# Kernel optimization log

Hardware: AMD Instinct MI355X
Metric: run time of the kernel (lower is better)

## Reference

```python
import jax, jax.numpy as jnp
import numpy as np

H = 768
F = 3072
NH = 12
EPS = 1e-5


def _layer_norm(x, g, b):
    mu = jnp.mean(x, axis=-1, keepdims=True)
    var = jnp.mean(jnp.square(x - mu), axis=-1, keepdims=True)
    return (x - mu) * jax.lax.rsqrt(var + EPS) * g + b


def setup_inputs() -> dict:
    key = jax.random.key(0)
    ks = jax.random.split(key, 16)
    s = 0.02
    d = {
        'x': jax.random.normal(ks[0], (2, 2048, H), jnp.float32),
        'Wq': jax.random.normal(ks[1], (H, H), jnp.float32) * s,
        'bq': jnp.zeros((H,), jnp.float32),
        'Wk': jax.random.normal(ks[2], (H, H), jnp.float32) * s,
        'bk': jnp.zeros((H,), jnp.float32),
        'Wv': jax.random.normal(ks[3], (H, H), jnp.float32) * s,
        'bv': jnp.zeros((H,), jnp.float32),
        'Wa1': jax.random.normal(ks[4], (H, H), jnp.float32) * s,
        'ba1': jnp.zeros((H,), jnp.float32),
        'g1': jnp.ones((H,), jnp.float32),
        'be1': jnp.zeros((H,), jnp.float32),
        'W1': jax.random.normal(ks[5], (H, F), jnp.float32) * s,
        'b1': jnp.zeros((F,), jnp.float32),
        'W2': jax.random.normal(ks[6], (F, H), jnp.float32) * s,
        'b2': jnp.zeros((H,), jnp.float32),
        'Wa2': jax.random.normal(ks[7], (H, H), jnp.float32) * s,
        'ba2': jnp.zeros((H,), jnp.float32),
        'g2': jnp.ones((H,), jnp.float32),
        'be2': jnp.zeros((H,), jnp.float32),
    }
    return d


def reference(x, Wq, bq, Wk, bk, Wv, bv, Wa1, ba1, g1, be1, W1, b1, W2, b2, Wa2, ba2, g2, be2):
    B, S, _ = x.shape
    Dh = H // NH
    # multi-head attention (naive: explicit scores + softmax)
    q = (x @ Wq + bq).reshape(B, S, NH, Dh)
    k = (x @ Wk + bk).reshape(B, S, NH, Dh)
    v = (x @ Wv + bv).reshape(B, S, NH, Dh)
    scores = jnp.einsum('bqhd,bkhd->bhqk', q, k) / jnp.sqrt(jnp.float32(Dh))
    att = jax.nn.softmax(scores, axis=-1)
    ctx = jnp.einsum('bhqk,bkhd->bqhd', att, v).reshape(B, S, H)
    # add_norm_1: Linear -> LayerNorm, then residual added AFTER LN (as in source)
    an1 = _layer_norm(ctx @ Wa1 + ba1, g1, be1) + x
    # feed-forward with exact GELU (torch nn.GELU default)
    ff = jax.nn.gelu(an1 @ W1 + b1, approximate=False) @ W2 + b2
    # add_norm_2: Linear -> LayerNorm, residual after LN
    out = _layer_norm(ff @ Wa2 + ba2, g2, be2) + an1
    return out
```

## Files before the change

kernel.cpp:

```cpp
#include <hip/hip_runtime.h>
#include <stdint.h>
#include <stddef.h>

#define HD 768
#define FF 3072
#define NHEAD 12
#define DHEAD 64
#define SEQ 2048
#define BATCH 2
#define NTOK (SEQ*BATCH)
#define SM_SCALE 0.18033688f

typedef __attribute__((ext_vector_type(8))) __bf16 bf16x8;
typedef __attribute__((ext_vector_type(4))) float f32x4;

__device__ __forceinline__ unsigned short f2bf(float f) {
  unsigned int u = __builtin_bit_cast(unsigned int, f);
  u += 0x7fffu + ((u >> 16) & 1u);
  return (unsigned short)(u >> 16);
}
__device__ __forceinline__ float bf2f(unsigned int s) {
  unsigned int u = s << 16;
  return __builtin_bit_cast(float, u);
}
__device__ __forceinline__ float4 ld4bf(const unsigned short* p) {
  uint2 w = *reinterpret_cast<const uint2*>(p);
  float4 o;
  o.x = bf2f(w.x & 0xffffu); o.y = bf2f(w.x >> 16);
  o.z = bf2f(w.y & 0xffffu); o.w = bf2f(w.y >> 16);
  return o;
}

__device__ __forceinline__ void gl16(const unsigned short* g, unsigned short* l) {
  __builtin_amdgcn_global_load_lds(
      (const __attribute__((address_space(1))) void*)g,
      (__attribute__((address_space(3))) void*)l,
      16, 0, 0);
}

__global__ void k_prep(const float* __restrict__ Wq, const float* __restrict__ Wk,
                       const float* __restrict__ Wv, const float* __restrict__ Wa1,
                       const float* __restrict__ W1, const float* __restrict__ W2,
                       const float* __restrict__ Wa2,
                       unsigned short* __restrict__ WqkvT, unsigned short* __restrict__ Wa1T,
                       unsigned short* __restrict__ W1T, unsigned short* __restrict__ W2T,
                       unsigned short* __restrict__ Wa2T,
                       const float* __restrict__ x, unsigned short* __restrict__ xb, int n4,
                       const float* __restrict__ bq, const float* __restrict__ bk,
                       const float* __restrict__ bv, float* __restrict__ biasqkv) {
  int t = blockIdx.x;
  int tid = threadIdx.x;
  if (t >= 7488) {
    int tb = t - 7488;
    if (tb < 9) {
      int idx = tb * 256 + tid;
      if (idx < 3*HD) {
        float v = idx < HD ? bq[idx] : idx < 2*HD ? bk[idx-HD] : bv[idx-2*HD];
        biasqkv[idx] = v;
      }
    }
    int i = tb * 256 + tid;
    int stride = 2048 * 256;
    for (; i < n4; i += stride) {
      float4 v = reinterpret_cast<const float4*>(x)[i];
      ushort4 o;
      o.x = f2bf(v.x); o.y = f2bf(v.y); o.z = f2bf(v.z); o.w = f2bf(v.w);
      reinterpret_cast<ushort4*>(xb)[i] = o;
    }
    return;
  }
  __shared__ float tile[32][33];
  const float* in; unsigned short* out; int K, N;
  if (t < 2304)      { int seg = t / 576; t -= seg * 576; K = HD; N = HD;
                       in  = seg==0 ? Wq : seg==1 ? Wk : seg==2 ? Wv : Wa1;
                       out = seg<3 ? WqkvT + seg*HD*HD : Wa1T; }
  else if (t < 4608) { t -= 2304; in = W1;  out = W1T;  K = HD; N = FF; }
  else if (t < 6912) { t -= 4608; in = W2;  out = W2T;  K = FF; N = HD; }
  else               { t -= 6912; in = Wa2; out = Wa2T; K = HD; N = HD; }
  int nt = N / 32;
  int nb = (t % nt) * 32, kb = (t / nt) * 32;
  int tx = tid & 31, ty = tid >> 5;
  for (int i = ty; i < 32; i += 8)
    tile[i][tx] = in[(size_t)(kb + i) * N + nb + tx];
  __syncthreads();
  for (int i = ty; i < 32; i += 8)
    out[(size_t)(nb + i) * K + kb + tx] = f2bf(tile[tx][i]);
}


#define BN 128
#define BK 64

template<int MODE, int TBM>
__global__ __launch_bounds__(256, 3)
void k_gemm(const unsigned short* __restrict__ A, const unsigned short* __restrict__ Bt,
            const float* __restrict__ bias, void* __restrict__ Cout,
            unsigned short* __restrict__ Vout,
            int M, int N, int K) {
  constexpr int MR = TBM / 32;
  constexpr int AI = TBM / 32;
  __shared__ unsigned short As[TBM*BK];
  __shared__ unsigned short Bs[BN*BK];
  int tid = threadIdx.x;
  int nwg = gridDim.x * gridDim.y;
  int lin = blockIdx.x + gridDim.x * blockIdx.y;
  int nl = (lin & 7) * (nwg >> 3) + (lin >> 3);
  int bm = (nl % gridDim.x) * TBM;
  int bn = (nl / gridDim.x) * BN;
  int wave = tid >> 6, lane = tid & 63;
  int wm = wave >> 1, wn = wave & 1;
  int wr = wm * (TBM/2);
  int wc = wn * 64;
  int fr = lane & 15;
  int hi = lane >> 4;

  f32x4 acc[MR][4];
#pragma unroll
  for (int m = 0; m < MR; ++m)
#pragma unroll
    for (int n = 0; n < 4; ++n) acc[m][n] = (f32x4){0.f,0.f,0.f,0.f};

  int g8 = lane >> 3;
  int cc = (lane & 7) ^ g8;
  int arow = (TBM/4)*wave + g8;
  int brow = 32*wave + g8;
  const unsigned short* ag = A + (size_t)(bm + arow) * K + cc*8;
  const unsigned short* bg = Bt + (size_t)(bn + brow) * K + cc*8;
  unsigned short* asl = As + (TBM/4)*wave*BK;
  unsigned short* bsl = Bs + 32*wave*BK;

  for (int k0 = 0; k0 < K; k0 += BK) {
#pragma unroll
    for (int i = 0; i < AI; ++i)
      gl16(ag + (size_t)(8*i)*K + k0, asl + (8*i)*BK);
#pragma unroll
    for (int i = 0; i < 4; ++i)
      gl16(bg + (size_t)(8*i)*K + k0, bsl + (8*i)*BK);
    __syncthreads();

    bf16x8 af[MR][2], bf[4][2];
#pragma unroll
    for (int m = 0; m < MR; ++m) {
      int R = wr + m*16 + fr, sw = R & 7;
#pragma unroll
      for (int h2 = 0; h2 < 2; ++h2)
        af[m][h2] = __builtin_bit_cast(bf16x8,
          *reinterpret_cast<const uint4*>(&As[R*BK + ((hi + h2*4) ^ sw)*8]));
    }
#pragma unroll
    for (int n = 0; n < 4; ++n) {
      int R = wc + n*16 + fr, sw = R & 7;
#pragma unroll
      for (int h2 = 0; h2 < 2; ++h2)
        bf[n][h2] = __builtin_bit_cast(bf16x8,
          *reinterpret_cast<const uint4*>(&Bs[R*BK + ((hi + h2*4) ^ sw)*8]));
    }
#pragma unroll
    for (int m = 0; m < MR; ++m)
#pragma unroll
      for (int n = 0; n < 4; ++n) {
        acc[m][n] = __builtin_amdgcn_mfma_f32_16x16x32_bf16(af[m][0], bf[n][0], acc[m][n], 0, 0, 0);
        acc[m][n] = __builtin_amdgcn_mfma_f32_16x16x32_bf16(af[m][1], bf[n][1], acc[m][n], 0, 0, 0);
      }
    __syncthreads();
  }

  int crow0 = (lane >> 4) * 4;
  int ccol = lane & 15;

  if (MODE == 3 && bn >= 2*HD) {
    unsigned short* tb = (wave < 2) ? As + wave*4096 : Bs + (wave-2)*4096;
#pragma unroll
    for (int m = 0; m < MR; ++m)
#pragma unroll
      for (int n = 0; n < 4; ++n)
#pragma unroll
        for (int r = 0; r < 4; ++r) {
          int tl = m*16 + crow0 + r;
          int cl = n*16 + ccol;
          float v = acc[m][n][r] + bias[bn + wc + cl];
          int pt = ((tl>>2)&3)*16 + ((tl>>4)<<2) + (tl&3);
          tb[cl*64 + (((pt>>3) ^ (cl&7))<<3) + (pt&7)] = f2bf(v);
        }
    __syncthreads();
    int tk0 = bm + wr;
    int bb = tk0 >> 11;
    int sb = tk0 & 2047;
    int hh = (bn + wc - 2*HD) >> 6;
    unsigned short* dst = Vout + ((size_t)(bb*NHEAD + hh) * DHEAD) * SEQ + sb;
#pragma unroll
    for (int p = 0; p < 8; ++p) {
      int dr = p*8 + (lane >> 3);
      int cj = lane & 7;
      uint4 w = *reinterpret_cast<const uint4*>(&tb[dr*64 + ((cj ^ (dr&7))<<3)]);
      *reinterpret_cast<uint4*>(dst + (size_t)dr*SEQ + cj*8) = w;
    }
    return;
  }

#pragma unroll
  for (int m = 0; m < MR; ++m) {
#pragma unroll
    for (int n = 0; n < 4; ++n) {
      int gcol = bn + wc + n*16 + ccol;
      float bv_ = bias[gcol];
#pragma unroll
      for (int r = 0; r < 4; ++r) {
        int grow = bm + wr + m*16 + crow0 + r;
        float v = acc[m][n][r] + bv_;
        if (MODE == 2) {
          float a = v + 0.044715f * v * v * v;
          v = v / (1.0f + exp2f(-2.3022082f * a));
        }
        if (MODE == 3 && gcol < HD) v *= SM_SCALE;
        reinterpret_cast<unsigned short*>(Cout)[(size_t)grow * N + gcol] = f2bf(v);
      }
    }
  }
}


#define KVB 128
#define KPK 72
#define KPV 136

__global__ __launch_bounds__(256, 3)
void k_attn_mfma(const unsigned short* __restrict__ qkv,
                 const unsigned short* __restrict__ vt,
                 unsigned short* __restrict__ ctx) {
  __shared__ __align__(16) char smem[40960];
  auto Ks = reinterpret_cast<unsigned short(*)[KPK]>(smem);
  auto Vt = reinterpret_cast<unsigned short(*)[KPV]>(smem + 18432);
  auto Mg = reinterpret_cast<f32x4(*)[64]>(smem);

  int tid = threadIdx.x;
  int wv = tid >> 6, lane = tid & 63;
  int lo = lane & 15, hi = lane >> 4;
  int qh = wv & 1;
  int kh = wv >> 1;

  int lin = blockIdx.x + 32*(blockIdx.y + NHEAD*blockIdx.z);
  int nl = (lin & 7) * 96 + (lin >> 3);
  int qb = nl & 31;
  int rest = nl >> 5;
  int h = rest % NHEAD;
  int b = rest / NHEAD;
  int q0 = qb * 64;

  for (int idx = tid; idx < 16*KPV; idx += 256) {
    int rr = idx / KPV, cc2 = idx - rr*KPV;
    Vt[64 + rr][cc2] = (rr == 0) ? (unsigned short)0x3F80 : (unsigned short)0;
  }

  const unsigned short* qpA = qkv + (size_t)(b*SEQ + q0 + qh*32 + lo) * 2304 + h*DHEAD + hi*8;
  const unsigned short* qpB = qpA + (size_t)16 * 2304;
  bf16x8 qfA0 = __builtin_bit_cast(bf16x8, *reinterpret_cast<const uint4*>(qpA));
  bf16x8 qfA1 = __builtin_bit_cast(bf16x8, *reinterpret_cast<const uint4*>(qpA + 32));
  bf16x8 qfB0 = __builtin_bit_cast(bf16x8, *reinterpret_cast<const uint4*>(qpB));
  bf16x8 qfB1 = __builtin_bit_cast(bf16x8, *reinterpret_cast<const uint4*>(qpB + 32));

  f32x4 poA[4], poB[4], po5A, po5B;
#pragma unroll
  for (int dt = 0; dt < 4; ++dt) { poA[dt] = (f32x4){0.f,0.f,0.f,0.f}; poB[dt] = (f32x4){0.f,0.f,0.f,0.f}; }
  po5A = (f32x4){0.f,0.f,0.f,0.f};
  po5B = (f32x4){0.f,0.f,0.f,0.f};

  int ksr = tid >> 1, kc = (tid & 1) * 32;
  int vdr = tid >> 2, vc = (tid & 3) * 32;
  const unsigned short* kgl = qkv + (size_t)(b*SEQ)*2304 + HD + h*DHEAD;
  const unsigned short* vgl = vt + ((size_t)(b*NHEAD + h)) * DHEAD * SEQ;

  for (int t0 = 0; t0 < SEQ; t0 += KVB) {
    const unsigned short* kp = kgl + (size_t)(t0 + ksr)*2304 + kc;
    const unsigned short* vp = vgl + (size_t)vdr*SEQ + t0 + vc;
    uint4 ku0 = *reinterpret_cast<const uint4*>(kp);
    uint4 ku1 = *reinterpret_cast<const uint4*>(kp + 8);
    uint4 ku2 = *reinterpret_cast<const uint4*>(kp + 16);
    uint4 ku3 = *reinterpret_cast<const uint4*>(kp + 24);
    uint4 vu0 = *reinterpret_cast<const uint4*>(vp);
    uint4 vu1 = *reinterpret_cast<const uint4*>(vp + 8);
    uint4 vu2 = *reinterpret_cast<const uint4*>(vp + 16);
    uint4 vu3 = *reinterpret_cast<const uint4*>(vp + 24);
    __syncthreads();
    *reinterpret_cast<uint4*>(&Ks[ksr][kc])      = ku0;
    *reinterpret_cast<uint4*>(&Ks[ksr][kc + 8])  = ku1;
    *reinterpret_cast<uint4*>(&Ks[ksr][kc + 16]) = ku2;
    *reinterpret_cast<uint4*>(&Ks[ksr][kc + 24]) = ku3;
    *reinterpret_cast<uint4*>(&Vt[vdr][vc])      = vu0;
    *reinterpret_cast<uint4*>(&Vt[vdr][vc + 8])  = vu1;
    *reinterpret_cast<uint4*>(&Vt[vdr][vc + 16]) = vu2;
    *reinterpret_cast<uint4*>(&Vt[vdr][vc + 24]) = vu3;
    __syncthreads();

    f32x4 sA[4], sB[4];
#pragma unroll
    for (int kg = 0; kg < 4; ++kg) {
      int krow = kh*64 + kg*16 + lo;
      bf16x8 a0 = __builtin_bit_cast(bf16x8, *reinterpret_cast<const uint4*>(&Ks[krow][hi*8]));
      bf16x8 a1 = __builtin_bit_cast(bf16x8, *reinterpret_cast<const uint4*>(&Ks[krow][32 + hi*8]));
      f32x4 s = (f32x4){0.f,0.f,0.f,0.f};
      s = __builtin_amdgcn_mfma_f32_16x16x32_bf16(a0, qfA0, s, 0, 0, 0);
      s = __builtin_amdgcn_mfma_f32_16x16x32_bf16(a1, qfA1, s, 0, 0, 0);
      sA[kg] = s;
      s = (f32x4){0.f,0.f,0.f,0.f};
      s = __builtin_amdgcn_mfma_f32_16x16x32_bf16(a0, qfB0, s, 0, 0, 0);
      s = __builtin_amdgcn_mfma_f32_16x16x32_bf16(a1, qfB1, s, 0, 0, 0);
      sB[kg] = s;
    }

    unsigned int pwA[8], pwB[8];
#pragma unroll
    for (int kg = 0; kg < 4; ++kg) {
      float a0 = exp2f(sA[kg][0]), a1 = exp2f(sA[kg][1]);
      float a2 = exp2f(sA[kg][2]), a3 = exp2f(sA[kg][3]);
      asm("v_cvt_pk_bf16_f32 %0, %1, %2" : "=v"(pwA[kg*2])   : "v"(a0), "v"(a1));
      asm("v_cvt_pk_bf16_f32 %0, %1, %2" : "=v"(pwA[kg*2+1]) : "v"(a2), "v"(a3));
      float b0 = exp2f(sB[kg][0]), b1 = exp2f(sB[kg][1]);
      float b2 = exp2f(sB[kg][2]), b3 = exp2f(sB[kg][3]);
      asm("v_cvt_pk_bf16_f32 %0, %1, %2" : "=v"(pwB[kg*2])   : "v"(b0), "v"(b1));
      asm("v_cvt_pk_bf16_f32 %0, %1, %2" : "=v"(pwB[kg*2+1]) : "v"(b2), "v"(b3));
    }

    uint4 uA0; uA0.x = pwA[0]; uA0.y = pwA[1]; uA0.z = pwA[2]; uA0.w = pwA[3];
    uint4 uA1; uA1.x = pwA[4]; uA1.y = pwA[5]; uA1.z = pwA[6]; uA1.w = pwA[7];
    uint4 uB0; uB0.x = pwB[0]; uB0.y = pwB[1]; uB0.z = pwB[2]; uB0.w = pwB[3];
    uint4 uB1; uB1.x = pwB[4]; uB1.y = pwB[5]; uB1.z = pwB[6]; uB1.w = pwB[7];
    bf16x8 paA0 = __builtin_bit_cast(bf16x8, uA0);
    bf16x8 paA1 = __builtin_bit_cast(bf16x8, uA1);
    bf16x8 paB0 = __builtin_bit_cast(bf16x8, uB0);
    bf16x8 paB1 = __builtin_bit_cast(bf16x8, uB1);

#pragma unroll
    for (int dt = 0; dt < 4; ++dt) {
      int col = dt*16 + lo;
      bf16x8 v0 = __builtin_bit_cast(bf16x8, *reinterpret_cast<const uint4*>(&Vt[col][kh*64 + hi*16]));
      bf16x8 v1 = __builtin_bit_cast(bf16x8, *reinterpret_cast<const uint4*>(&Vt[col][kh*64 + hi*16 + 8]));
      poA[dt] = __builtin_amdgcn_mfma_f32_16x16x32_bf16(paA0, v0, poA[dt], 0, 0, 0);
      poA[dt] = __builtin_amdgcn_mfma_f32_16x16x32_bf16(paA1, v1, poA[dt], 0, 0, 0);
      poB[dt] = __builtin_amdgcn_mfma_f32_16x16x32_bf16(paB0, v0, poB[dt], 0, 0, 0);
      poB[dt] = __builtin_amdgcn_mfma_f32_16x16x32_bf16(paB1, v1, poB[dt], 0, 0, 0);
    }
    {
      bf16x8 o0 = __builtin_bit_cast(bf16x8, *reinterpret_cast<const uint4*>(&Vt[64 + lo][kh*64 + hi*16]));
      bf16x8 o1 = __builtin_bit_cast(bf16x8, *reinterpret_cast<const uint4*>(&Vt[64 + lo][kh*64 + hi*16 + 8]));
      po5A = __builtin_amdgcn_mfma_f32_16x16x32_bf16(paA0, o0, po5A, 0, 0, 0);
      po5A = __builtin_amdgcn_mfma_f32_16x16x32_bf16(paA1, o1, po5A, 0, 0, 0);
      po5B = __builtin_amdgcn_mfma_f32_16x16x32_bf16(paB0, o0, po5B, 0, 0, 0);
      po5B = __builtin_amdgcn_mfma_f32_16x16x32_bf16(paB1, o1, po5B, 0, 0, 0);
    }
  }

  __syncthreads();
  if (kh == 1) {
#pragma unroll
    for (int dt = 0; dt < 4; ++dt) {
      Mg[qh*10 + dt][lane] = poA[dt];
      Mg[qh*10 + 4 + dt][lane] = poB[dt];
    }
    Mg[qh*10 + 8][lane] = po5A;
    Mg[qh*10 + 9][lane] = po5B;
  }
  __syncthreads();
  if (kh == 0) {
#pragma unroll
    for (int dt = 0; dt < 4; ++dt) {
      f32x4 mA = Mg[qh*10 + dt][lane], mB = Mg[qh*10 + 4 + dt][lane];
      poA[dt][0] += mA[0]; poA[dt][1] += mA[1]; poA[dt][2] += mA[2]; poA[dt][3] += mA[3];
      poB[dt][0] += mB[0]; poB[dt][1] += mB[1]; poB[dt][2] += mB[2]; poB[dt][3] += mB[3];
    }
    f32x4 m5A = Mg[qh*10 + 8][lane], m5B = Mg[qh*10 + 9][lane];
    po5A[0] += m5A[0]; po5A[1] += m5A[1]; po5A[2] += m5A[2]; po5A[3] += m5A[3];
    po5B[0] += m5B[0]; po5B[1] += m5B[1]; po5B[2] += m5B[2]; po5B[3] += m5B[3];

    unsigned short* op = ctx + (size_t)(b*SEQ + q0 + qh*32) * HD + h*DHEAD;
#pragma unroll
    for (int r = 0; r < 4; ++r) {
      float LA = __shfl(po5A[r], hi*16);
      float LB = __shfl(po5B[r], hi*16);
      float liA = (LA > 0.f) ? 1.0f / LA : 0.f;
      float liB = (LB > 0.f) ? 1.0f / LB : 0.f;
      int row = hi*4 + r;
#pragma unroll
      for (int dt = 0; dt < 4; ++dt) {
        op[(size_t)row*HD + dt*16 + lo]        = f2bf(poA[dt][r] * liA);
        op[(size_t)(16 + row)*HD + dt*16 + lo] = f2bf(poB[dt][r] * liB);
      }
    }
  }
}

template<int RESID_BF16, int WRITE_F32>
__global__ __launch_bounds__(256, 4)
void k_ln(const unsigned short* __restrict__ xin, const void* __restrict__ resid_,
          const float* __restrict__ g, const float* __restrict__ be,
          float* __restrict__ outf, unsigned short* __restrict__ outb) {
  int wave = threadIdx.x >> 6, lane = threadIdx.x & 63;
  int row = blockIdx.x * 4 + wave;
  const unsigned short* xp = xin + (size_t)row * HD;
  const float4* gp = reinterpret_cast<const float4*>(g);
  const float4* bp = reinterpret_cast<const float4*>(be);
  float4 v[3];
  float sum = 0.f, sq = 0.f;
#pragma unroll
  for (int i = 0; i < 3; ++i) {
    v[i] = ld4bf(xp + (lane + 64*i)*4);
    sum += v[i].x + v[i].y + v[i].z + v[i].w;
    sq  += v[i].x*v[i].x + v[i].y*v[i].y + v[i].z*v[i].z + v[i].w*v[i].w;
  }
#pragma unroll
  for (int m = 1; m < 64; m <<= 1) { sum += __shfl_xor(sum, m); sq += __shfl_xor(sq, m); }
  float mean = sum * (1.0f/768.0f);
  float var = sq * (1.0f/768.0f) - mean*mean;
  float rstd = rsqrtf(var + 1e-5f);
#pragma unroll
  for (int i = 0; i < 3; ++i) {
    float4 gg = gp[lane + 64*i], bb = bp[lane + 64*i];
    float4 rr;
    if (RESID_BF16)
      rr = ld4bf((const unsigned short*)resid_ + (size_t)row * HD + (lane + 64*i)*4);
    else
      rr = reinterpret_cast<const float4*>((const float*)resid_ + (size_t)row * HD)[lane + 64*i];
    float4 o;
    o.x = (v[i].x - mean)*rstd*gg.x + bb.x + rr.x;
    o.y = (v[i].y - mean)*rstd*gg.y + bb.y + rr.y;
    o.z = (v[i].z - mean)*rstd*gg.z + bb.z + rr.z;
    o.w = (v[i].w - mean)*rstd*gg.w + bb.w + rr.w;
    if (WRITE_F32) {
      reinterpret_cast<float4*>(outf + (size_t)row * HD)[lane + 64*i] = o;
    } else {
      ushort4 ob;
      ob.x = f2bf(o.x); ob.y = f2bf(o.y); ob.z = f2bf(o.z); ob.w = f2bf(o.w);
      reinterpret_cast<ushort4*>(outb + (size_t)row * HD)[lane + 64*i] = ob;
    }
  }
}


extern "C" void kernel_launch(void* const* d_in, const int* in_sizes, int n_in,
                              void* d_out, int out_size, void* d_ws, size_t ws_size,
                              hipStream_t stream) {
  const float* x   = (const float*)d_in[0];
  const float* Wq  = (const float*)d_in[1];
  const float* bq  = (const float*)d_in[2];
  const float* Wk  = (const float*)d_in[3];
  const float* bk  = (const float*)d_in[4];
  const float* Wv  = (const float*)d_in[5];
  const float* bv  = (const float*)d_in[6];
  const float* Wa1 = (const float*)d_in[7];
  const float* ba1 = (const float*)d_in[8];
  const float* g1  = (const float*)d_in[9];
  const float* be1 = (const float*)d_in[10];
  const float* W1  = (const float*)d_in[11];
  const float* b1  = (const float*)d_in[12];
  const float* W2  = (const float*)d_in[13];
  const float* b2  = (const float*)d_in[14];
  const float* Wa2 = (const float*)d_in[15];
  const float* ba2 = (const float*)d_in[16];
  const float* g2  = (const float*)d_in[17];
  const float* be2 = (const float*)d_in[18];

  char* ws = (char*)d_ws;
  size_t off = 0;
  auto alloc = [&](size_t bytes) -> void* {
    void* p = ws + off;
    off += (bytes + 255) & ~(size_t)255;
    return p;
  };
  unsigned short* xb    = (unsigned short*)alloc((size_t)NTOK*HD*2);
  unsigned short* WqkvT = (unsigned short*)alloc((size_t)3*HD*HD*2);
  unsigned short* Wa1T  = (unsigned short*)alloc((size_t)HD*HD*2);
  unsigned short* W1T   = (unsigned short*)alloc((size_t)FF*HD*2);
  unsigned short* W2T   = (unsigned short*)alloc((size_t)HD*FF*2);
  unsigned short* Wa2T  = (unsigned short*)alloc((size_t)HD*HD*2);
  float*          biasqkv = (float*)alloc((size_t)3*HD*4);
  unsigned short* qkvb  = (unsigned short*)alloc((size_t)NTOK*3*HD*2);
  unsigned short* vtb   = (unsigned short*)alloc((size_t)NTOK*HD*2);
  unsigned short* ctxb  = (unsigned short*)alloc((size_t)NTOK*HD*2);
  unsigned short* a1b   = (unsigned short*)alloc((size_t)NTOK*HD*2);
  unsigned short* an1b  = (unsigned short*)alloc((size_t)NTOK*HD*2);
  unsigned short* h1g   = (unsigned short*)alloc((size_t)NTOK*FF*2);
  unsigned short* f2b   = (unsigned short*)alloc((size_t)NTOK*HD*2);
  unsigned short* a2b   = (unsigned short*)alloc((size_t)NTOK*HD*2);
  (void)ws_size; (void)in_sizes; (void)n_in; (void)out_size;

  k_prep<<<9536, 256, 0, stream>>>(Wq, Wk, Wv, Wa1, W1, W2, Wa2,
                                   WqkvT, Wa1T, W1T, W2T, Wa2T,
                                   x, xb, NTOK*HD/4, bq, bk, bv, biasqkv);

  k_gemm<3,128><<<dim3(NTOK/128, 2304/BN), 256, 0, stream>>>(xb, WqkvT, biasqkv, qkvb, vtb, NTOK, 3*HD, HD);
  k_attn_mfma<<<dim3(SEQ/64, NHEAD, BATCH), 256, 0, stream>>>(qkvb, vtb, ctxb);
  k_gemm<1,64><<<dim3(NTOK/64, HD/BN), 256, 0, stream>>>(ctxb, Wa1T, ba1, a1b, nullptr, NTOK, HD, HD);
  k_ln<0,0><<<NTOK/4, 256, 0, stream>>>(a1b, x, g1, be1, nullptr, an1b);
  k_gemm<2,128><<<dim3(NTOK/128, FF/BN), 256, 0, stream>>>(an1b, W1T, b1, h1g, nullptr, NTOK, FF, HD);
  k_gemm<1,64><<<dim3(NTOK/64, HD/BN), 256, 0, stream>>>(h1g, W2T, b2, f2b, nullptr, NTOK, HD, FF);
  k_gemm<1,64><<<dim3(NTOK/64, HD/BN), 256, 0, stream>>>(f2b, Wa2T, ba2, a2b, nullptr, NTOK, HD, HD);
  k_ln<1,1><<<NTOK/4, 256, 0, stream>>>(a2b, an1b, g2, be2, (float*)d_out, nullptr);
}
```

Before: 189.9 us.

## Give each attention wave its own query rows over full KV tile

The attention kernel now assigns each of the four waves 32 distinct query rows (128 queries per block), and each wave walks both 64-key halves of every KV tile itself. Previously two waves split the keys and had to merge partial outputs through shared memory. This removes the cross-wave reduction and its barriers, and halves how often each K/V tile is loaded per query. The cost is half as many blocks (384), which may leave the GPU's compute units underfilled, plus twice the per-wave work inside each tile.

```diff
diff --git a/kernel.cpp b/kernel.cpp
--- a/kernel.cpp
+++ b/kernel.cpp
@@ -228,31 +228,28 @@
 void k_attn_mfma(const unsigned short* __restrict__ qkv,
                  const unsigned short* __restrict__ vt,
                  unsigned short* __restrict__ ctx) {
-  __shared__ __align__(16) char smem[40960];
+  __shared__ __align__(16) char smem[40192];
   auto Ks = reinterpret_cast<unsigned short(*)[KPK]>(smem);
   auto Vt = reinterpret_cast<unsigned short(*)[KPV]>(smem + 18432);
-  auto Mg = reinterpret_cast<f32x4(*)[64]>(smem);
 
   int tid = threadIdx.x;
   int wv = tid >> 6, lane = tid & 63;
   int lo = lane & 15, hi = lane >> 4;
-  int qh = wv & 1;
-  int kh = wv >> 1;
-
-  int lin = blockIdx.x + 32*(blockIdx.y + NHEAD*blockIdx.z);
-  int nl = (lin & 7) * 96 + (lin >> 3);
-  int qb = nl & 31;
-  int rest = nl >> 5;
+
+  int lin = blockIdx.x + 16*(blockIdx.y + NHEAD*blockIdx.z);
+  int nl = (lin & 7) * 48 + (lin >> 3);
+  int qb = nl & 15;
+  int rest = nl >> 4;
   int h = rest % NHEAD;
   int b = rest / NHEAD;
-  int q0 = qb * 64;
+  int q0 = qb * 128;
 
   for (int idx = tid; idx < 16*KPV; idx += 256) {
     int rr = idx / KPV, cc2 = idx - rr*KPV;
     Vt[64 + rr][cc2] = (rr == 0) ? (unsigned short)0x3F80 : (unsigned short)0;
   }
 
-  const unsigned short* qpA = qkv + (size_t)(b*SEQ + q0 + qh*32 + lo) * 2304 + h*DHEAD + hi*8;
+  const unsigned short* qpA = qkv + (size_t)(b*SEQ + q0 + wv*32 + lo) * 2304 + h*DHEAD + hi*8;
   const unsigned short* qpB = qpA + (size_t)16 * 2304;
   bf16x8 qfA0 = __builtin_bit_cast(bf16x8, *reinterpret_cast<const uint4*>(qpA));
   bf16x8 qfA1 = __builtin_bit_cast(bf16x8, *reinterpret_cast<const uint4*>(qpA + 32));
@@ -292,99 +289,79 @@
     *reinterpret_cast<uint4*>(&Vt[vdr][vc + 24]) = vu3;
     __syncthreads();
 
-    f32x4 sA[4], sB[4];
-#pragma unroll
-    for (int kg = 0; kg < 4; ++kg) {
-      int krow = kh*64 + kg*16 + lo;
-      bf16x8 a0 = __builtin_bit_cast(bf16x8, *reinterpret_cast<const uint4*>(&Ks[krow][hi*8]));
-      bf16x8 a1 = __builtin_bit_cast(bf16x8, *reinterpret_cast<const uint4*>(&Ks[krow][32 + hi*8]));
-      f32x4 s = (f32x4){0.f,0.f,0.f,0.f};
-      s = __builtin_amdgcn_mfma_f32_16x16x32_bf16(a0, qfA0, s, 0, 0, 0);
-      s = __builtin_amdgcn_mfma_f32_16x16x32_bf16(a1, qfA1, s, 0, 0, 0);
-      sA[kg] = s;
-      s = (f32x4){0.f,0.f,0.f,0.f};
-      s = __builtin_amdgcn_mfma_f32_16x16x32_bf16(a0, qfB0, s, 0, 0, 0);
-      s = __builtin_amdgcn_mfma_f32_16x16x32_bf16(a1, qfB1, s, 0, 0, 0);
-      sB[kg] = s;
-    }
-
-    unsigned int pwA[8], pwB[8];
-#pragma unroll
-    for (int kg = 0; kg < 4; ++kg) {
-      float a0 = exp2f(sA[kg][0]), a1 = exp2f(sA[kg][1]);
-      float a2 = exp2f(sA[kg][2]), a3 = exp2f(sA[kg][3]);
-      asm("v_cvt_pk_bf16_f32 %0, %1, %2" : "=v"(pwA[kg*2])   : "v"(a0), "v"(a1));
-      asm("v_cvt_pk_bf16_f32 %0, %1, %2" : "=v"(pwA[kg*2+1]) : "v"(a2), "v"(a3));
-      float b0 = exp2f(sB[kg][0]), b1 = exp2f(sB[kg][1]);
-      float b2 = exp2f(sB[kg][2]), b3 = exp2f(sB[kg][3]);
-      asm("v_cvt_pk_bf16_f32 %0, %1, %2" : "=v"(pwB[kg*2])   : "v"(b0), "v"(b1));
-      asm("v_cvt_pk_bf16_f32 %0, %1, %2" : "=v"(pwB[kg*2+1]) : "v"(b2), "v"(b3));
-    }
-
-    uint4 uA0; uA0.x = pwA[0]; uA0.y = pwA[1]; uA0.z = pwA[2]; uA0.w = pwA[3];
-    uint4 uA1; uA1.x = pwA[4]; uA1.y = pwA[5]; uA1.z = pwA[6]; uA1.w = pwA[7];
-    uint4 uB0; uB0.x = pwB[0]; uB0.y = pwB[1]; uB0.z = pwB[2]; uB0.w = pwB[3];
-    uint4 uB1; uB1.x = pwB[4]; uB1.y = pwB[5]; uB1.z = pwB[6]; uB1.w = pwB[7];
-    bf16x8 paA0 = __builtin_bit_cast(bf16x8, uA0);
-    bf16x8 paA1 = __builtin_bit_cast(bf16x8, uA1);
-    bf16x8 paB0 = __builtin_bit_cast(bf16x8, uB0);
-    bf16x8 paB1 = __builtin_bit_cast(bf16x8, uB1);
-
+#pragma unroll
+    for (int hh = 0; hh < 2; ++hh) {
+      f32x4 sA[4], sB[4];
+#pragma unroll
+      for (int kg = 0; kg < 4; ++kg) {
+        int krow = hh*64 + kg*16 + lo;
+        bf16x8 a0 = __builtin_bit_cast(bf16x8, *reinterpret_cast<const uint4*>(&Ks[krow][hi*8]));
+        bf16x8 a1 = __builtin_bit_cast(bf16x8, *reinterpret_cast<const uint4*>(&Ks[krow][32 + hi*8]));
+        f32x4 s = (f32x4){0.f,0.f,0.f,0.f};
+        s = __builtin_amdgcn_mfma_f32_16x16x32_bf16(a0, qfA0, s, 0, 0, 0);
+        s = __builtin_amdgcn_mfma_f32_16x16x32_bf16(a1, qfA1, s, 0, 0, 0);
+        sA[kg] = s;
+        s = (f32x4){0.f,0.f,0.f,0.f};
+        s = __builtin_amdgcn_mfma_f32_16x16x32_bf16(a0, qfB0, s, 0, 0, 0);
+        s = __builtin_amdgcn_mfma_f32_16x16x32_bf16(a1, qfB1, s, 0, 0, 0);
+        sB[kg] = s;
+      }
+
+      unsigned int pwA[8], pwB[8];
+#pragma unroll
+      for (int kg = 0; kg < 4; ++kg) {
+        float a0 = exp2f(sA[kg][0]), a1 = exp2f(sA[kg][1]);
+        float a2 = exp2f(sA[kg][2]), a3 = exp2f(sA[kg][3]);
+        asm("v_cvt_pk_bf16_f32 %0, %1, %2" : "=v"(pwA[kg*2])   : "v"(a0), "v"(a1));
+        asm("v_cvt_pk_bf16_f32 %0, %1, %2" : "=v"(pwA[kg*2+1]) : "v"(a2), "v"(a3));
+        float b0 = exp2f(sB[kg][0]), b1 = exp2f(sB[kg][1]);
+        float b2 = exp2f(sB[kg][2]), b3 = exp2f(sB[kg][3]);
+        asm("v_cvt_pk_bf16_f32 %0, %1, %2" : "=v"(pwB[kg*2])   : "v"(b0), "v"(b1));
+        asm("v_cvt_pk_bf16_f32 %0, %1, %2" : "=v"(pwB[kg*2+1]) : "v"(b2), "v"(b3));
+      }
+
+      uint4 uA0; uA0.x = pwA[0]; uA0.y = pwA[1]; uA0.z = pwA[2]; uA0.w = pwA[3];
+      uint4 uA1; uA1.x = pwA[4]; uA1.y = pwA[5]; uA1.z = pwA[6]; uA1.w = pwA[7];
+      uint4 uB0; uB0.x = pwB[0]; uB0.y = pwB[1]; uB0.z = pwB[2]; uB0.w = pwB[3];
+      uint4 uB1; uB1.x = pwB[4]; uB1.y = pwB[5]; uB1.z = pwB[6]; uB1.w = pwB[7];
+      bf16x8 paA0 = __builtin_bit_cast(bf16x8, uA0);
+      bf16x8 paA1 = __builtin_bit_cast(bf16x8, uA1);
+      bf16x8 paB0 = __builtin_bit_cast(bf16x8, uB0);
+      bf16x8 paB1 = __builtin_bit_cast(bf16x8, uB1);
+
+#pragma unroll
+      for (int dt = 0; dt < 4; ++dt) {
+        int col = dt*16 + lo;
+        bf16x8 v0 = __builtin_bit_cast(bf16x8, *reinterpret_cast<const uint4*>(&Vt[col][hh*64 + hi*16]));
+        bf16x8 v1 = __builtin_bit_cast(bf16x8, *reinterpret_cast<const uint4*>(&Vt[col][hh*64 + hi*16 + 8]));
+        poA[dt] = __builtin_amdgcn_mfma_f32_16x16x32_bf16(paA0, v0, poA[dt], 0, 0, 0);
+        poA[dt] = __builtin_amdgcn_mfma_f32_16x16x32_bf16(paA1, v1, poA[dt], 0, 0, 0);
+        poB[dt] = __builtin_amdgcn_mfma_f32_16x16x32_bf16(paB0, v0, poB[dt], 0, 0, 0);
+        poB[dt] = __builtin_amdgcn_mfma_f32_16x16x32_bf16(paB1, v1, poB[dt], 0, 0, 0);
+      }
+      {
+        bf16x8 o0 = __builtin_bit_cast(bf16x8, *reinterpret_cast<const uint4*>(&Vt[64 + lo][hh*64 + hi*16]));
+        bf16x8 o1 = __builtin_bit_cast(bf16x8, *reinterpret_cast<const uint4*>(&Vt[64 + lo][hh*64 + hi*16 + 8]));
+        po5A = __builtin_amdgcn_mfma_f32_16x16x32_bf16(paA0, o0, po5A, 0, 0, 0);
+        po5A = __builtin_amdgcn_mfma_f32_16x16x32_bf16(paA1, o1, po5A, 0, 0, 0);
+        po5B = __builtin_amdgcn_mfma_f32_16x16x32_bf16(paB0, o0, po5B, 0, 0, 0);
+        po5B = __builtin_amdgcn_mfma_f32_16x16x32_bf16(paB1, o1, po5B, 0, 0, 0);
+      }
+    }
+  }
+
+  unsigned short* op = ctx + (size_t)(b*SEQ + q0 + wv*32) * HD + h*DHEAD;
+#pragma unroll
+  for (int r = 0; r < 4; ++r) {
+    float LA = __shfl(po5A[r], hi*16);
+    float LB = __shfl(po5B[r], hi*16);
+    float liA = (LA > 0.f) ? 1.0f / LA : 0.f;
+    float liB = (LB > 0.f) ? 1.0f / LB : 0.f;
+    int row = hi*4 + r;
 #pragma unroll
     for (int dt = 0; dt < 4; ++dt) {
-      int col = dt*16 + lo;
-      bf16x8 v0 = __builtin_bit_cast(bf16x8, *reinterpret_cast<const uint4*>(&Vt[col][kh*64 + hi*16]));
-      bf16x8 v1 = __builtin_bit_cast(bf16x8, *reinterpret_cast<const uint4*>(&Vt[col][kh*64 + hi*16 + 8]));
-      poA[dt] = __builtin_amdgcn_mfma_f32_16x16x32_bf16(paA0, v0, poA[dt], 0, 0, 0);
-      poA[dt] = __builtin_amdgcn_mfma_f32_16x16x32_bf16(paA1, v1, poA[dt], 0, 0, 0);
-      poB[dt] = __builtin_amdgcn_mfma_f32_16x16x32_bf16(paB0, v0, poB[dt], 0, 0, 0);
-      poB[dt] = __builtin_amdgcn_mfma_f32_16x16x32_bf16(paB1, v1, poB[dt], 0, 0, 0);
-    }
-    {
-      bf16x8 o0 = __builtin_bit_cast(bf16x8, *reinterpret_cast<const uint4*>(&Vt[64 + lo][kh*64 + hi*16]));
-      bf16x8 o1 = __builtin_bit_cast(bf16x8, *reinterpret_cast<const uint4*>(&Vt[64 + lo][kh*64 + hi*16 + 8]));
-      po5A = __builtin_amdgcn_mfma_f32_16x16x32_bf16(paA0, o0, po5A, 0, 0, 0);
-      po5A = __builtin_amdgcn_mfma_f32_16x16x32_bf16(paA1, o1, po5A, 0, 0, 0);
-      po5B = __builtin_amdgcn_mfma_f32_16x16x32_bf16(paB0, o0, po5B, 0, 0, 0);
-      po5B = __builtin_amdgcn_mfma_f32_16x16x32_bf16(paB1, o1, po5B, 0, 0, 0);
-    }
-  }
-
-  __syncthreads();
-  if (kh == 1) {
-#pragma unroll
-    for (int dt = 0; dt < 4; ++dt) {
-      Mg[qh*10 + dt][lane] = poA[dt];
-      Mg[qh*10 + 4 + dt][lane] = poB[dt];
-    }
-    Mg[qh*10 + 8][lane] = po5A;
-    Mg[qh*10 + 9][lane] = po5B;
-  }
-  __syncthreads();
-  if (kh == 0) {
-#pragma unroll
-    for (int dt = 0; dt < 4; ++dt) {
-      f32x4 mA = Mg[qh*10 + dt][lane], mB = Mg[qh*10 + 4 + dt][lane];
-      poA[dt][0] += mA[0]; poA[dt][1] += mA[1]; poA[dt][2] += mA[2]; poA[dt][3] += mA[3];
-      poB[dt][0] += mB[0]; poB[dt][1] += mB[1]; poB[dt][2] += mB[2]; poB[dt][3] += mB[3];
-    }
-    f32x4 m5A = Mg[qh*10 + 8][lane], m5B = Mg[qh*10 + 9][lane];
-    po5A[0] += m5A[0]; po5A[1] += m5A[1]; po5A[2] += m5A[2]; po5A[3] += m5A[3];
-    po5B[0] += m5B[0]; po5B[1] += m5B[1]; po5B[2] += m5B[2]; po5B[3] += m5B[3];
-
-    unsigned short* op = ctx + (size_t)(b*SEQ + q0 + qh*32) * HD + h*DHEAD;
-#pragma unroll
-    for (int r = 0; r < 4; ++r) {
-      float LA = __shfl(po5A[r], hi*16);
-      float LB = __shfl(po5B[r], hi*16);
-      float liA = (LA > 0.f) ? 1.0f / LA : 0.f;
-      float liB = (LB > 0.f) ? 1.0f / LB : 0.f;
-      int row = hi*4 + r;
-#pragma unroll
-      for (int dt = 0; dt < 4; ++dt) {
-        op[(size_t)row*HD + dt*16 + lo]        = f2bf(poA[dt][r] * liA);
-        op[(size_t)(16 + row)*HD + dt*16 + lo] = f2bf(poB[dt][r] * liB);
-      }
+      op[(size_t)row*HD + dt*16 + lo]        = f2bf(poA[dt][r] * liA);
+      op[(size_t)(16 + row)*HD + dt*16 + lo] = f2bf(poB[dt][r] * liB);
     }
   }
 }
@@ -488,7 +465,7 @@
                                    x, xb, NTOK*HD/4, bq, bk, bv, biasqkv);
 
   k_gemm<3,128><<<dim3(NTOK/128, 2304/BN), 256, 0, stream>>>(xb, WqkvT, biasqkv, qkvb, vtb, NTOK, 3*HD, HD);
-  k_attn_mfma<<<dim3(SEQ/64, NHEAD, BATCH), 256, 0, stream>>>(qkvb, vtb, ctxb);
+  k_attn_mfma<<<dim3(SEQ/128, NHEAD, BATCH), 256, 0, stream>>>(qkvb, vtb, ctxb);
   k_gemm<1,64><<<dim3(NTOK/64, HD/BN), 256, 0, stream>>>(ctxb, Wa1T, ba1, a1b, nullptr, NTOK, HD, HD);
   k_ln<0,0><<<NTOK/4, 256, 0, stream>>>(a1b, x, g1, be1, nullptr, an1b);
   k_gemm<2,128><<<dim3(NTOK/128, FF/BN), 256, 0, stream>>>(an1b, W1T, b1, h1g, nullptr, NTOK, FF, HD);
```

New measurement: 203.8 us. 1.07x slower.
